# Optimization experiments

Measured on AMD Instinct MI355X. Metric: run time of the kernel, lower is better.

## Reference

```python
import jax, jax.numpy as jnp
import numpy as np

B, S, H = 2, 256, 256
R = H  # rdim defaults to hidden_size


def setup_inputs() -> dict:
    key = jax.random.key(0)
    k1, k2, k3 = jax.random.split(key, 3)
    hidden_states = jax.random.normal(k1, (B, S, H), dtype=jnp.float32)
    # Linear weights stored torch-style [out, in]
    Wqkv = jax.random.normal(k2, (3 * R, H), dtype=jnp.float32) * (H ** -0.5)
    bqkv = jnp.zeros((3 * R,), dtype=jnp.float32)
    Wc = jax.random.normal(k3, (R, R), dtype=jnp.float32) * (R ** -0.5)
    bc = jnp.zeros((R,), dtype=jnp.float32)
    return {"hidden_states": hidden_states, "Wqkv": Wqkv, "bqkv": bqkv, "Wc": Wc, "bc": bc}


def reference(hidden_states, Wqkv, bqkv, Wc, bc):
    # qkv projection: [B,S,3R]
    qkv = jnp.einsum('bsh,rh->bsr', hidden_states, Wqkv) + bqkv
    q, k, v = jnp.split(qkv, 3, axis=-1)  # each [B,S,R]
    # Tucker-style outer-product scores: [B,S,L,R]
    scores = jnp.einsum('bsr,blr->bslr', q, k)
    # c_proj mixes the r dimension
    scores = jnp.einsum('bslr,pr->bslp', scores, Wc) + bc
    # rearrange 'b s l r -> (b r) s l' + softmax(dim=-1) == softmax over l axis
    probs = jax.nn.softmax(scores, axis=2)
    # 'brsl,blr->bsr' after rearrange back == 'bslr,blr->bsr'
    return jnp.einsum('bslr,blr->bsr', probs, v)
```

## Files before the change

### kernel.cpp

```cpp
#include <hip/hip_runtime.h>
#include <hip/hip_bf16.h>
#include <math.h>

typedef __bf16 bf16;
typedef _Float16 f16;
typedef __attribute__((ext_vector_type(8))) __bf16 bf16x8;
typedef __attribute__((ext_vector_type(8))) _Float16 f16x8;
typedef __attribute__((ext_vector_type(4))) _Float16 f16x4;
typedef __attribute__((ext_vector_type(4))) float floatx4;

#define MFMA16(a, b, c) __builtin_amdgcn_mfma_f32_16x16x16f16(a, b, c, 0, 0, 0)

__device__ __forceinline__ void split8(floatx4 a0, floatx4 a1, bf16x8& hi, bf16x8& lo) {
#pragma unroll
    for (int t = 0; t < 4; t++) {
        float v0 = a0[t], v1 = a1[t];
        bf16 h0 = (bf16)v0, h1 = (bf16)v1;
        hi[t] = h0;     lo[t] = (bf16)(v0 - (float)h0);
        hi[t + 4] = h1; lo[t + 4] = (bf16)(v1 - (float)h1);
    }
}

__global__ __launch_bounds__(256, 4)
void proj_kernel(const float* __restrict__ hs, const float* __restrict__ Wq,
                 const float* __restrict__ bq, const float* __restrict__ Wc,
                 f16* __restrict__ q_ws, f16* __restrict__ k_ws,
                 f16* __restrict__ vT_ws, f16* __restrict__ Wc_ws)
{
    const int tid = threadIdx.x;
    if (blockIdx.x >= 384) {
        const int base = (blockIdx.x - 384) * 1024 + tid * 4;
        floatx4 w = *(const floatx4*)(Wc + base);
        f16x4 h;
        h.x = (f16)w.x; h.y = (f16)w.y; h.z = (f16)w.z; h.w = (f16)w.w;
        *(f16x4*)(Wc_ws + base) = h;
        return;
    }
    const int wv = tid >> 6, lane = tid & 63;
    const int quad = lane >> 4, lcol = lane & 15;
    const int wt = blockIdx.x * 4 + wv;
    const int rt = wt / 48, ct = wt - rt * 48;
    const int row0 = rt * 16, col0 = ct * 16;

    const float* arow = hs + (row0 + lcol) * 256;
    const float* brow = Wq + (col0 + lcol) * 256;

    floatx4 acc = {0.f, 0.f, 0.f, 0.f};
#pragma unroll
    for (int ks = 0; ks < 8; ks++) {
        const int h = ks * 32 + quad * 8;
        floatx4 a0 = *(const floatx4*)(arow + h);
        floatx4 a1 = *(const floatx4*)(arow + h + 4);
        floatx4 b0 = *(const floatx4*)(brow + h);
        floatx4 b1 = *(const floatx4*)(brow + h + 4);
        bf16x8 ahi, alo, bhi, blo;
        split8(a0, a1, ahi, alo);
        split8(b0, b1, bhi, blo);
        acc = __builtin_amdgcn_mfma_f32_16x16x32_bf16(ahi, bhi, acc, 0, 0, 0);
        acc = __builtin_amdgcn_mfma_f32_16x16x32_bf16(ahi, blo, acc, 0, 0, 0);
        acc = __builtin_amdgcn_mfma_f32_16x16x32_bf16(alo, bhi, acc, 0, 0, 0);
    }
    const float bias = bq[col0 + lcol];
    const int col = col0 + lcol, seg = col0 >> 8, jj = col & 255;
#pragma unroll
    for (int r = 0; r < 4; r++) {
        const int row = row0 + quad * 4 + r;
        const float val = acc[r] + bias;
        if (seg == 0)      q_ws[row * 256 + jj] = (f16)val;
        else if (seg == 1) k_ws[row * 256 + jj] = (f16)val;
        else               vT_ws[(row >> 8) * 65536 + jj * 256 + (row & 255)] = (f16)val;
    }
}

__global__ __launch_bounds__(512, 2)
void attn_main(const f16* __restrict__ qw, const f16* __restrict__ kw,
               const f16* __restrict__ vT, const f16* __restrict__ Wc16,
               float* __restrict__ out)
{
    __shared__ f16 Klds[256 * 256];
    __shared__ f16 Plds[8 * 64 * 24];
    __shared__ float obuf[4][2][64];
    __shared__ float sbuf[4][2][64];

    const int bid = blockIdx.x;
    const int pt = bid & 3;
    const int sg = (bid >> 2) & 31;
    const int b  = bid >> 7;
    const int p0 = pt * 64;
    const int tid  = threadIdx.x;
    const int wv   = tid >> 6;
    const int lane = tid & 63;
    const int quad = lane >> 4, lcol = lane & 15;
    const int lq = wv & 3, sh = wv >> 2;
    const int l0w = lq * 64;

    const f16* kbase = kw + b * 65536;
    const f16* vbase = vT + b * 65536;

#pragma unroll
    for (int it = 0; it < 16; it++) {
        const int id = tid + it * 512;
        const int l = id >> 5, c = id & 31;
        const int csrc = c ^ (l & 7);
        uint4 d = *(const uint4*)(kbase + l * 256 + csrc * 8);
        *(uint4*)(Klds + l * 256 + c * 8) = d;
    }

    f16x4 vfrag[4][4];
#pragma unroll
    for (int d = 0; d < 4; d++)
#pragma unroll
        for (int c = 0; c < 4; c++)
            vfrag[d][c] = *(const f16x4*)(vbase + (p0 + d * 16 + lcol) * 256 + l0w + c * 16 + quad * 4);

    f16x4 ones4;
#pragma unroll
    for (int t = 0; t < 4; t++) ones4[t] = (f16)1.0f;

    __syncthreads();

    f16* Pw = Plds + wv * 1536;

    for (int sl = 0; sl < 4; sl++) {
        const int s = sg * 8 + sh * 4 + sl;
        const f16* qrow = qw + (b * 256 + s) * 256;

        floatx4 acc[4][4];
#pragma unroll
        for (int i = 0; i < 4; i++)
#pragma unroll
            for (int j = 0; j < 4; j++)
                acc[i][j] = (floatx4){0.f, 0.f, 0.f, 0.f};

#pragma unroll
        for (int kk = 0; kk < 8; kk++) {
            const int rb = kk * 32 + quad * 8;
            f16x8 qv = *(const f16x8*)(qrow + rb);
            f16x8 kf[4];
#pragma unroll
            for (int i = 0; i < 4; i++)
                kf[i] = *(const f16x8*)(Klds + (l0w + i * 16 + lcol) * 256 +
                                        (((kk * 4 + quad) ^ (lcol & 7)) << 3));
#pragma unroll
            for (int j = 0; j < 4; j++) {
                f16x8 wv8 = *(const f16x8*)(Wc16 + (p0 + j * 16 + lcol) * 256 + rb);
                f16x8 bf = wv8 * qv;
#pragma unroll
                for (int i = 0; i < 4; i++)
                    acc[i][j] = __builtin_amdgcn_mfma_f32_16x16x32_f16(kf[i], bf, acc[i][j], 0, 0, 0);
            }
        }

        floatx4 co[4], cs[4];
#pragma unroll
        for (int d = 0; d < 4; d++) {
            co[d] = (floatx4){0.f, 0.f, 0.f, 0.f};
            cs[d] = (floatx4){0.f, 0.f, 0.f, 0.f};
        }
#pragma unroll
        for (int c = 0; c < 4; c++) {
#pragma unroll
            for (int j = 0; j < 4; j++) {
                f16x4 pv;
#pragma unroll
                for (int r = 0; r < 4; r++)
                    pv[r] = (f16)__expf(acc[c][j][r]);
                *(f16x4*)(Pw + (j * 16 + lcol) * 24 + quad * 4) = pv;
            }
#pragma unroll
            for (int d = 0; d < 4; d++) {
                f16x4 pa = *(const f16x4*)(Pw + (d * 16 + lcol) * 24 + quad * 4);
                co[d] = MFMA16(pa, vfrag[d][c], co[d]);
                cs[d] = MFMA16(pa, ones4, cs[d]);
            }
        }

        if ((lcol >> 2) == quad) {
            const int r = lcol & 3;
#pragma unroll
            for (int d = 0; d < 4; d++) {
                obuf[lq][sh][d * 16 + lcol] = co[d][r];
                sbuf[lq][sh][d * 16 + lcol] = cs[d][r];
            }
        }
        __syncthreads();
        if (tid < 128) {
            const int ss = tid >> 6, p = tid & 63;
            const float O = obuf[0][ss][p] + obuf[1][ss][p] + obuf[2][ss][p] + obuf[3][ss][p];
            const float S = sbuf[0][ss][p] + sbuf[1][ss][p] + sbuf[2][ss][p] + sbuf[3][ss][p];
            out[(b * 256 + sg * 8 + ss * 4 + sl) * 256 + p0 + p] = O / S;
        }
        __syncthreads();
    }
}

extern "C" void kernel_launch(void* const* d_in, const int* in_sizes, int n_in,
                              void* d_out, int out_size, void* d_ws, size_t ws_size,
                              hipStream_t stream) {
    const float* hs   = (const float*)d_in[0];
    const float* Wqkv = (const float*)d_in[1];
    const float* bqkv = (const float*)d_in[2];
    const float* Wc   = (const float*)d_in[3];
    float* out = (float*)d_out;

    char* ws = (char*)d_ws;
    f16* q_ws   = (f16*)ws;
    f16* k_ws   = (f16*)(ws + 262144);
    f16* vT_ws  = (f16*)(ws + 524288);
    f16* Wc_ws  = (f16*)(ws + 786432);

    proj_kernel<<<dim3(448), 256, 0, stream>>>(hs, Wqkv, bqkv, Wc, q_ws, k_ws, vT_ws, Wc_ws);
    attn_main<<<dim3(256), 512, 0, stream>>>(q_ws, k_ws, vT_ws, Wc_ws, out);
}
```

Before: 106.9 us.

## Stage Wc slice in LDS, read K from global, and double the grid

The attention kernel now keeps the block's 64-row slice of Wc in shared memory (32KB) and reads K fragments straight from global/L2, instead of staging the full 128KB K tile in LDS. Each block handles 4 rows instead of 8 and the grid doubles to 512 blocks, with launch bounds raised to allow more resident blocks. The P·V product and row sums move from an LDS round-trip plus MFMA to scalar FMAs with lane shuffles, and a single end-of-kernel sync replaces the per-row syncs. This trades LDS capacity and MFMA work for more global K and V traffic and extra VALU work, aiming for better occupancy and fewer barriers.

```diff
diff --git a/kernel.cpp b/kernel.cpp
--- a/kernel.cpp
+++ b/kernel.cpp
@@ -8,8 +8,6 @@
 typedef __attribute__((ext_vector_type(8))) _Float16 f16x8;
 typedef __attribute__((ext_vector_type(4))) _Float16 f16x4;
 typedef __attribute__((ext_vector_type(4))) float floatx4;
-
-#define MFMA16(a, b, c) __builtin_amdgcn_mfma_f32_16x16x16f16(a, b, c, 0, 0, 0)
 
 __device__ __forceinline__ void split8(floatx4 a0, floatx4 a1, bf16x8& hi, bf16x8& lo) {
 #pragma unroll
@@ -72,20 +70,19 @@
     }
 }
 
-__global__ __launch_bounds__(512, 2)
+__global__ __launch_bounds__(512, 4)
 void attn_main(const f16* __restrict__ qw, const f16* __restrict__ kw,
                const f16* __restrict__ vT, const f16* __restrict__ Wc16,
                float* __restrict__ out)
 {
-    __shared__ f16 Klds[256 * 256];
-    __shared__ f16 Plds[8 * 64 * 24];
-    __shared__ float obuf[4][2][64];
-    __shared__ float sbuf[4][2][64];
+    __shared__ f16 Wlds[64 * 256];
+    __shared__ float obuf[4][4][64];
+    __shared__ float sbuf[4][4][64];
 
     const int bid = blockIdx.x;
     const int pt = bid & 3;
-    const int sg = (bid >> 2) & 31;
-    const int b  = bid >> 7;
+    const int sg = (bid >> 2) & 63;
+    const int b  = bid >> 8;
     const int p0 = pt * 64;
     const int tid  = threadIdx.x;
     const int wv   = tid >> 6;
@@ -98,31 +95,20 @@
     const f16* vbase = vT + b * 65536;
 
 #pragma unroll
-    for (int it = 0; it < 16; it++) {
+    for (int it = 0; it < 4; it++) {
         const int id = tid + it * 512;
-        const int l = id >> 5, c = id & 31;
-        const int csrc = c ^ (l & 7);
-        uint4 d = *(const uint4*)(kbase + l * 256 + csrc * 8);
-        *(uint4*)(Klds + l * 256 + c * 8) = d;
-    }
-
-    f16x4 vfrag[4][4];
-#pragma unroll
-    for (int d = 0; d < 4; d++)
-#pragma unroll
-        for (int c = 0; c < 4; c++)
-            vfrag[d][c] = *(const f16x4*)(vbase + (p0 + d * 16 + lcol) * 256 + l0w + c * 16 + quad * 4);
-
-    f16x4 ones4;
-#pragma unroll
-    for (int t = 0; t < 4; t++) ones4[t] = (f16)1.0f;
-
+        const int r = id >> 5, c = id & 31;
+        const int csrc = c ^ (r & 7);
+        uint4 d = *(const uint4*)(Wc16 + (p0 + r) * 256 + csrc * 8);
+        *(uint4*)(Wlds + r * 256 + c * 8) = d;
+    }
     __syncthreads();
 
-    f16* Pw = Plds + wv * 1536;
-
-    for (int sl = 0; sl < 4; sl++) {
-        const int s = sg * 8 + sh * 4 + sl;
+    float osum[2][4], ssum[2][4];
+
+#pragma unroll
+    for (int sl = 0; sl < 2; sl++) {
+        const int s = sg * 4 + sh * 2 + sl;
         const f16* qrow = qw + (b * 256 + s) * 256;
 
         floatx4 acc[4][4];
@@ -139,58 +125,59 @@
             f16x8 kf[4];
 #pragma unroll
             for (int i = 0; i < 4; i++)
-                kf[i] = *(const f16x8*)(Klds + (l0w + i * 16 + lcol) * 256 +
-                                        (((kk * 4 + quad) ^ (lcol & 7)) << 3));
+                kf[i] = *(const f16x8*)(kbase + (l0w + i * 16 + lcol) * 256 + rb);
 #pragma unroll
             for (int j = 0; j < 4; j++) {
-                f16x8 wv8 = *(const f16x8*)(Wc16 + (p0 + j * 16 + lcol) * 256 + rb);
-                f16x8 bf = wv8 * qv;
+                f16x8 w8 = *(const f16x8*)(Wlds + (j * 16 + lcol) * 256 +
+                                           (((kk * 4 + quad) ^ (lcol & 7)) << 3));
+                f16x8 bfr = w8 * qv;
 #pragma unroll
                 for (int i = 0; i < 4; i++)
-                    acc[i][j] = __builtin_amdgcn_mfma_f32_16x16x32_f16(kf[i], bf, acc[i][j], 0, 0, 0);
+                    acc[i][j] = __builtin_amdgcn_mfma_f32_16x16x32_f16(kf[i], bfr, acc[i][j], 0, 0, 0);
             }
         }
 
-        floatx4 co[4], cs[4];
-#pragma unroll
-        for (int d = 0; d < 4; d++) {
-            co[d] = (floatx4){0.f, 0.f, 0.f, 0.f};
-            cs[d] = (floatx4){0.f, 0.f, 0.f, 0.f};
-        }
-#pragma unroll
-        for (int c = 0; c < 4; c++) {
+        float os[4] = {0.f, 0.f, 0.f, 0.f}, ss[4] = {0.f, 0.f, 0.f, 0.f};
+#pragma unroll
+        for (int i = 0; i < 4; i++) {
 #pragma unroll
             for (int j = 0; j < 4; j++) {
-                f16x4 pv;
-#pragma unroll
-                for (int r = 0; r < 4; r++)
-                    pv[r] = (f16)__expf(acc[c][j][r]);
-                *(f16x4*)(Pw + (j * 16 + lcol) * 24 + quad * 4) = pv;
-            }
-#pragma unroll
-            for (int d = 0; d < 4; d++) {
-                f16x4 pa = *(const f16x4*)(Pw + (d * 16 + lcol) * 24 + quad * 4);
-                co[d] = MFMA16(pa, vfrag[d][c], co[d]);
-                cs[d] = MFMA16(pa, ones4, cs[d]);
+                f16x4 vf = *(const f16x4*)(vbase + (p0 + j * 16 + lcol) * 256 + l0w + i * 16 + quad * 4);
+#pragma unroll
+                for (int t = 0; t < 4; t++) {
+                    const float P = __expf(acc[i][j][t]);
+                    os[j] = fmaf(P, (float)vf[t], os[j]);
+                    ss[j] += P;
+                }
             }
         }
-
-        if ((lcol >> 2) == quad) {
-            const int r = lcol & 3;
-#pragma unroll
-            for (int d = 0; d < 4; d++) {
-                obuf[lq][sh][d * 16 + lcol] = co[d][r];
-                sbuf[lq][sh][d * 16 + lcol] = cs[d][r];
+#pragma unroll
+        for (int j = 0; j < 4; j++) {
+            os[j] += __shfl_xor(os[j], 16);
+            os[j] += __shfl_xor(os[j], 32);
+            ss[j] += __shfl_xor(ss[j], 16);
+            ss[j] += __shfl_xor(ss[j], 32);
+            osum[sl][j] = os[j];
+            ssum[sl][j] = ss[j];
+        }
+    }
+
+    if (quad == 0) {
+#pragma unroll
+        for (int sl = 0; sl < 2; sl++)
+#pragma unroll
+            for (int j = 0; j < 4; j++) {
+                obuf[lq][sh * 2 + sl][j * 16 + lcol] = osum[sl][j];
+                sbuf[lq][sh * 2 + sl][j * 16 + lcol] = ssum[sl][j];
             }
-        }
-        __syncthreads();
-        if (tid < 128) {
-            const int ss = tid >> 6, p = tid & 63;
-            const float O = obuf[0][ss][p] + obuf[1][ss][p] + obuf[2][ss][p] + obuf[3][ss][p];
-            const float S = sbuf[0][ss][p] + sbuf[1][ss][p] + sbuf[2][ss][p] + sbuf[3][ss][p];
-            out[(b * 256 + sg * 8 + ss * 4 + sl) * 256 + p0 + p] = O / S;
-        }
-        __syncthreads();
+    }
+    __syncthreads();
+
+    if (tid < 256) {
+        const int slot = tid >> 6, p = tid & 63;
+        const float O = obuf[0][slot][p] + obuf[1][slot][p] + obuf[2][slot][p] + obuf[3][slot][p];
+        const float S = sbuf[0][slot][p] + sbuf[1][slot][p] + sbuf[2][slot][p] + sbuf[3][slot][p];
+        out[(b * 256 + sg * 4 + slot) * 256 + p0 + p] = O / S;
     }
 }
 
@@ -210,5 +197,5 @@
     f16* Wc_ws  = (f16*)(ws + 786432);
 
     proj_kernel<<<dim3(448), 256, 0, stream>>>(hs, Wqkv, bqkv, Wc, q_ws, k_ws, vT_ws, Wc_ws);
-    attn_main<<<dim3(256), 512, 0, stream>>>(q_ws, k_ws, vT_ws, Wc_ws, out);
-}
+    attn_main<<<dim3(512), 512, 0, stream>>>(q_ws, k_ws, vT_ws, Wc_ws, out);
+}
```

Result: slower. 249.6 us (+133.4%).
